# Kernel optimization log

Hardware: AMD Instinct MI355X
Metric: run time of the kernel (lower is better)

## Reference

```python
import jax, jax.numpy as jnp
import numpy as np

B, T, C_IN = 2, 4096, 1024
INTER, OUT = 1024, 1024
ROPE_DIM = 64
GAMMA = 0.99609375  # 1 - 2**-8
GROUPS = 32
EPS = 1e-6


def setup_inputs() -> dict:
    key = jax.random.key(0)
    k = jax.random.split(key, 4)
    return {
        "X_Q": jax.random.normal(k[0], (B, T, C_IN), dtype=jnp.float32),
        "W_Q": jax.random.normal(k[1], (C_IN, INTER), dtype=jnp.float32) / C_IN,
        "W_K": jax.random.normal(k[2], (C_IN, INTER), dtype=jnp.float32) / C_IN,
        "W_V": jax.random.normal(k[3], (C_IN, OUT), dtype=jnp.float32) / C_IN,
        "gn_weight": jnp.ones((OUT,), dtype=jnp.float32),
        "gn_bias": jnp.zeros((OUT,), dtype=jnp.float32),
    }


def _rope(x):
    # lucidrains RotaryEmbedding: rotate first ROPE_DIM features, pairwise-adjacent
    t = x.shape[-2]
    inv_freq = 1.0 / (10000.0 ** (jnp.arange(0, ROPE_DIM, 2, dtype=jnp.float32) / ROPE_DIM))
    freqs = jnp.arange(t, dtype=jnp.float32)[:, None] * inv_freq[None, :]  # [T, ROPE_DIM/2]
    freqs = jnp.repeat(freqs, 2, axis=-1)                                   # [T, ROPE_DIM]
    cos, sin = jnp.cos(freqs), jnp.sin(freqs)
    xr, xp = x[..., :ROPE_DIM], x[..., ROPE_DIM:]
    x1, x2 = xr[..., 0::2], xr[..., 1::2]
    rot = jnp.stack([-x2, x1], axis=-1).reshape(xr.shape)  # rotate_half (adjacent pairs)
    return jnp.concatenate([xr * cos + rot * sin, xp], axis=-1)


def _group_norm(x, w, b):
    # torch GroupNorm applied on x.reshape(-1, C)
    sh = x.shape
    c = sh[-1]
    xr = x.reshape(-1, GROUPS, c // GROUPS)
    mu = xr.mean(-1, keepdims=True)
    var = xr.var(-1, keepdims=True)
    xn = ((xr - mu) * jax.lax.rsqrt(var + EPS)).reshape(-1, c)
    return (xn * w + b).reshape(sh)


def reference(X_Q, W_Q, W_K, W_V, gn_weight, gn_bias):
    Q = jax.nn.silu(_rope(X_Q @ W_Q))  # [B,T,INTER]
    K = jax.nn.silu(_rope(X_Q @ W_K))
    V = jax.nn.silu(X_Q @ W_V)         # [B,T,OUT]
    A = jnp.einsum('btd,bsd->bts', Q, K)  # [B,T,T]
    # decay mask: original multiplies by _get_D(gamma,T).T -> gamma^(m-n) for m>=n
    n = jnp.arange(T)[:, None]
    m = jnp.arange(T)[None, :]
    upper = m >= n
    Dt = jnp.where(upper, GAMMA ** jnp.where(upper, m - n, 0).astype(jnp.float32), 0.0)
    A = A * Dt
    out = jnp.einsum('bts,bsd->btd', A, V)  # [B,T,OUT]
    # dropout p=0 (eval) -> identity
    return _group_norm(out, gn_weight, gn_bias)
```

## Files before the change

### kernel.cpp

```cpp
#include <hip/hip_runtime.h>


typedef __attribute__((ext_vector_type(8))) short bf16x8;
typedef __attribute__((ext_vector_type(4))) short bf16x4;
typedef __attribute__((ext_vector_type(4))) float f32x4;

#define MFMA16(a, b, c) __builtin_amdgcn_mfma_f32_16x16x32_bf16(a, b, c, 0, 0, 0)

static __device__ __forceinline__ short f2bf(float f) {
  unsigned u = __builtin_bit_cast(unsigned, f);
  u = (u + 0x7fffu + ((u >> 16) & 1u)) >> 16;
  return (short)u;
}

static __device__ __forceinline__ void gl_lds16(const void* g, void* l) {
  __builtin_amdgcn_global_load_lds(
      (const __attribute__((address_space(1))) void*)g,
      (__attribute__((address_space(3))) void*)l, 16, 0, 0);
}

static __device__ __forceinline__ int swzc(int col, int row) {
  return (((col >> 3) ^ (row & 7)) << 3) | (col & 7);
}

#define T_LEN 4096
#define CIN 1024

#define LOG2G (-0.0056465633f)
#define L2IF (0.41524101f)

__global__ __launch_bounds__(256)
void convert_x(const float* __restrict__ X, short* __restrict__ Xb) {
  const int gid = blockIdx.x * 256 + threadIdx.x;
  const int row = gid >> 7;
  const int c = gid & 127;
  const float* s = &X[(size_t)gid * 8];
  float4 f0 = *(const float4*)s;
  float4 f1 = *(const float4*)(s + 4);
  bf16x8 v = {f2bf(f0.x), f2bf(f0.y), f2bf(f0.z), f2bf(f0.w),
              f2bf(f1.x), f2bf(f1.y), f2bf(f1.z), f2bf(f1.w)};
  const int pc = (c & 0x78) | ((c ^ row) & 7);
  *(bf16x8*)&Xb[(size_t)row * 1024 + pc * 8] = v;
}

__global__ __launch_bounds__(256)
void transpose_w(const float* __restrict__ Wq, const float* __restrict__ Wk,
                 const float* __restrict__ Wv, short* __restrict__ WT) {
  const int k0 = blockIdx.x * 64, n0 = blockIdx.y * 64, mat = blockIdx.z;
  const float* __restrict__ W = (mat == 0) ? Wq : (mat == 1) ? Wk : Wv;
  __shared__ short tile[64][72];
  const int tid = threadIdx.x;
  const int r = tid >> 4, c = tid & 15;
#pragma unroll
  for (int i = 0; i < 4; ++i) {
    int row = r + 16 * i;
    float4 f = *(const float4*)&W[(size_t)(k0 + row) * CIN + n0 + c * 4];
    tile[c * 4 + 0][row] = f2bf(f.x);
    tile[c * 4 + 1][row] = f2bf(f.y);
    tile[c * 4 + 2][row] = f2bf(f.z);
    tile[c * 4 + 3][row] = f2bf(f.w);
  }
  __syncthreads();
  const int n = tid >> 2, seg = tid & 3;
  bf16x8 lo = *(const bf16x8*)&tile[n][seg * 16];
  bf16x8 hi = *(const bf16x8*)&tile[n][seg * 16 + 8];
  const int R = mat * 1024 + n0 + n;
  const int a0 = (k0 >> 3) + seg * 2;
  short* base = &WT[(size_t)R * CIN];
  *(bf16x8*)&base[(a0 ^ (n & 7)) * 8] = lo;
  *(bf16x8*)&base[((a0 + 1) ^ (n & 7)) * 8] = hi;
}

#define GEMM_DECLS()                                   \
  const int tid = threadIdx.x;                         \
  const int lane = tid & 63, wave = tid >> 6;          \
  const int wm = wave >> 1, wn = wave & 1;             \
  const int l15 = lane & 15, quad = lane >> 4;         \
  const int srow = tid >> 3;                           \
  const int scol = (tid & 7) * 8;                      \
  const int asw = (l15 & 7);

#define ACC_INIT4(acc)                                 \
  _Pragma("unroll") for (int i = 0; i < 4; ++i)        \
  _Pragma("unroll") for (int j = 0; j < 4; ++j) {      \
    f32x4 z = {0.f, 0.f, 0.f, 0.f};                    \
    acc[i][j] = z;                                     \
  }

#define STAGE_TILE(dst, src, ld, r0, k0, nrows)        \
  _Pragma("unroll") for (int i = 0; i < (nrows) / 32; ++i) \
    gl_lds16(&src[(size_t)((r0) + i * 32 + srow) * (ld) + (k0) + scol], \
             &dst[i * 32 + srow][scol]);

#define FRAG_MFMA44(As, Bs, acc)                                            \
  {                                                                         \
    bf16x8 af[4][2], bfr[4][2];                                             \
    _Pragma("unroll") for (int im = 0; im < 4; ++im)                        \
    _Pragma("unroll") for (int ks = 0; ks < 2; ++ks)                        \
      af[im][ks] = *(const bf16x8*)&As[wm * 64 + im * 16 + l15]             \
                       [((ks * 4 + quad) ^ asw) * 8];                       \
    _Pragma("unroll") for (int in = 0; in < 4; ++in)                        \
    _Pragma("unroll") for (int ks = 0; ks < 2; ++ks)                        \
      bfr[in][ks] = *(const bf16x8*)&Bs[wn * 64 + in * 16 + l15]            \
                        [((ks * 4 + quad) ^ asw) * 8];                      \
    _Pragma("unroll") for (int ks = 0; ks < 2; ++ks)                        \
    _Pragma("unroll") for (int im = 0; im < 4; ++im)                        \
    _Pragma("unroll") for (int in = 0; in < 4; ++in)                        \
      acc[im][in] = MFMA16(af[im][ks], bfr[in][ks], acc[im][in]);           \
  }

__global__ __launch_bounds__(256, 2)
void qkv_gemm(const short* __restrict__ Xb, const short* __restrict__ WT,
              short* __restrict__ Qb, short* __restrict__ Kb,
              short* __restrict__ Vt) {
  __shared__ __align__(16) short As[128][64];
  __shared__ __align__(16) short Bs[128][64];
  GEMM_DECLS();
  const int m0 = blockIdx.x * 128;
  const int c0 = blockIdx.y * 128;

  f32x4 acc[4][4];
  ACC_INIT4(acc);

  for (int k0 = 0; k0 < CIN; k0 += 64) {
    __syncthreads();
    STAGE_TILE(As, Xb, CIN, m0, k0, 128);
    STAGE_TILE(Bs, WT, CIN, c0, k0, 128);
    __syncthreads();
    FRAG_MFMA44(As, Bs, acc);
  }

  const int mat = (c0 >> 10);
#pragma unroll
  for (int im = 0; im < 4; ++im) {
#pragma unroll
    for (int in = 0; in < 4; ++in) {
      const int c = c0 + wn * 64 + in * 16 + l15;
      const int colm = c & 1023;
      const bool rope = (mat < 2) && (colm < 64);
      const float invf = exp2f(-L2IF * (float)(colm >> 1));
      const int mbase = m0 + wm * 64 + im * 16 + quad * 4;
      short vv[4];
#pragma unroll
      for (int r = 0; r < 4; ++r) {
        float v = acc[im][in][r];
        int m = mbase + r;
        int t = m & (T_LEN - 1);
        float partner = __shfl_xor(v, 1, 64);
        if (rope) {
          float ang = (float)t * invf;
          float s_, c_;
          sincosf(ang, &s_, &c_);
          v = (colm & 1) ? (v * c_ + partner * s_) : (v * c_ - partner * s_);
        }
        v = v / (1.f + __expf(-v));
        vv[r] = f2bf(v);
      }
      if (mat == 0) {
#pragma unroll
        for (int r = 0; r < 4; ++r)
          Qb[(size_t)(mbase + r) * 1024 + swzc(colm, mbase + r)] = vv[r];
      } else if (mat == 1) {
#pragma unroll
        for (int r = 0; r < 4; ++r)
          Kb[(size_t)(mbase + r) * 1024 + swzc(colm, mbase + r)] = vv[r];
      } else {
        bf16x4 v4 = {vv[0], vv[1], vv[2], vv[3]};
        *(bf16x4*)&Vt[(size_t)colm * 8192 +
                      (((mbase >> 3) ^ (colm & 7)) << 3) + (mbase & 7)] = v4;
      }
    }
  }
}

__global__ __launch_bounds__(256, 2)
void score_kernel(const short* __restrict__ Qb, const short* __restrict__ Kb,
                  short* __restrict__ Ab) {
  int idx = blockIdx.x;
  int ti = 0;
  while (idx >= 32 - ti) { idx -= 32 - ti; ++ti; }
  const int si = ti + idx;
  const int b = blockIdx.y;
  const int s0 = si * 128, t0 = ti * 128;

  __shared__ __align__(16) short Qs[128][64];
  __shared__ __align__(16) short Ks[128][64];
  GEMM_DECLS();

  f32x4 acc[4][4];
  ACC_INIT4(acc);

  for (int k0 = 0; k0 < 1024; k0 += 64) {
    __syncthreads();
    STAGE_TILE(Qs, Qb, 1024, b * T_LEN + t0, k0, 128);
    STAGE_TILE(Ks, Kb, 1024, b * T_LEN + s0, k0, 128);
    __syncthreads();
    FRAG_MFMA44(Qs, Ks, acc);
  }

#pragma unroll
  for (int im = 0; im < 4; ++im) {
#pragma unroll
    for (int in = 0; in < 4; ++in) {
      int s = s0 + wn * 64 + in * 16 + l15;
#pragma unroll
      for (int r = 0; r < 4; ++r) {
        int t = t0 + wm * 64 + im * 16 + quad * 4 + r;
        int d = s - t;
        float v = acc[im][in][r];
        v = (d < 0) ? 0.f : v * exp2f((float)d * LOG2G);
        Ab[((size_t)(b * T_LEN + t)) * T_LEN + swzc(s, t)] = f2bf(v);
      }
    }
  }
}

__global__ __launch_bounds__(256, 2)
void av_kernel(const short* __restrict__ Ab, const short* __restrict__ Vt,
               float* __restrict__ Out) {
  const int p = blockIdx.x, b = blockIdx.y, di = blockIdx.z;
  const int n0 = di * 128;

  __shared__ __align__(16) short As2[64][64];
  __shared__ __align__(16) short Vs[128][64];
  GEMM_DECLS();

#pragma unroll 1
  for (int half = 0; half < 2; ++half) {
    const int ti2 = half ? (63 - p) : p;
    const int t0 = ti2 * 64;

    f32x4 acc[2][4];
#pragma unroll
    for (int i = 0; i < 2; ++i)
#pragma unroll
      for (int j = 0; j < 4; ++j) {
        f32x4 z = {0.f, 0.f, 0.f, 0.f};
        acc[i][j] = z;
      }

    for (int s = t0; s < T_LEN; s += 64) {
      __syncthreads();
      STAGE_TILE(As2, Ab, T_LEN, b * T_LEN + t0, s, 64);
      STAGE_TILE(Vs, Vt, 8192, n0, b * T_LEN + s, 128);
      __syncthreads();
      bf16x8 af[2][2], bfr[4][2];
#pragma unroll
      for (int im = 0; im < 2; ++im)
#pragma unroll
        for (int ks = 0; ks < 2; ++ks)
          af[im][ks] = *(const bf16x8*)&As2[wm * 32 + im * 16 + l15]
                           [((ks * 4 + quad) ^ asw) * 8];
#pragma unroll
      for (int in = 0; in < 4; ++in)
#pragma unroll
        for (int ks = 0; ks < 2; ++ks)
          bfr[in][ks] = *(const bf16x8*)&Vs[wn * 64 + in * 16 + l15]
                            [((ks * 4 + quad) ^ asw) * 8];
#pragma unroll
      for (int ks = 0; ks < 2; ++ks)
#pragma unroll
        for (int im = 0; im < 2; ++im)
#pragma unroll
          for (int in = 0; in < 4; ++in)
            acc[im][in] = MFMA16(af[im][ks], bfr[in][ks], acc[im][in]);
    }

#pragma unroll
    for (int im = 0; im < 2; ++im) {
#pragma unroll
      for (int in = 0; in < 4; ++in) {
        int n = n0 + wn * 64 + in * 16 + l15;
#pragma unroll
        for (int r = 0; r < 4; ++r) {
          int t = t0 + wm * 32 + im * 16 + quad * 4 + r;
          Out[((size_t)(b * T_LEN + t)) * 1024 + n] = acc[im][in][r];
        }
      }
    }
  }
}

__global__ __launch_bounds__(256)
void gn_kernel(float* __restrict__ Out, const float* __restrict__ gw,
               const float* __restrict__ gb) {
  const int row = blockIdx.x;
  const int tid = threadIdx.x;
  const int ch0 = tid * 4;
  float4 v = *(const float4*)&Out[(size_t)row * 1024 + ch0];
  float s = v.x + v.y + v.z + v.w;
  float q = v.x * v.x + v.y * v.y + v.z * v.z + v.w * v.w;
  s += __shfl_xor(s, 1, 64);
  q += __shfl_xor(q, 1, 64);
  s += __shfl_xor(s, 2, 64);
  q += __shfl_xor(q, 2, 64);
  s += __shfl_xor(s, 4, 64);
  q += __shfl_xor(q, 4, 64);
  float mean = s * (1.f / 32.f);
  float var = q * (1.f / 32.f) - mean * mean;
  float rstd = rsqrtf(var + 1e-6f);
  float4 o;
  o.x = (v.x - mean) * rstd * gw[ch0 + 0] + gb[ch0 + 0];
  o.y = (v.y - mean) * rstd * gw[ch0 + 1] + gb[ch0 + 1];
  o.z = (v.z - mean) * rstd * gw[ch0 + 2] + gb[ch0 + 2];
  o.w = (v.w - mean) * rstd * gw[ch0 + 3] + gb[ch0 + 3];
  *(float4*)&Out[(size_t)row * 1024 + ch0] = o;
}

extern "C" void kernel_launch(void* const* d_in, const int* in_sizes, int n_in,
                              void* d_out, int out_size, void* d_ws,
                              size_t ws_size, hipStream_t stream) {
  const float* X = (const float*)d_in[0];
  const float* Wq = (const float*)d_in[1];
  const float* Wk = (const float*)d_in[2];
  const float* Wv = (const float*)d_in[3];
  const float* gw = (const float*)d_in[4];
  const float* gb = (const float*)d_in[5];
  float* Out = (float*)d_out;

  short* Qb = (short*)d_ws;
  short* Kb = Qb + (size_t)8192 * 1024;
  short* Vt = Kb + (size_t)8192 * 1024;
  short* Ab = Vt + (size_t)8192 * 1024;
  short* Xb = Ab;
  short* WT = Xb + (size_t)8192 * 1024;

  convert_x<<<4096, 256, 0, stream>>>(X, Xb);
  transpose_w<<<dim3(16, 16, 3), 256, 0, stream>>>(Wq, Wk, Wv, WT);
  qkv_gemm<<<dim3(64, 24), 256, 0, stream>>>(Xb, WT, Qb, Kb, Vt);
  score_kernel<<<dim3(528, 2), 256, 0, stream>>>(Qb, Kb, Ab);
  av_kernel<<<dim3(32, 2, 8), 256, 0, stream>>>(Ab, Vt, Out);
  gn_kernel<<<8192, 256, 0, stream>>>(Out, gw, gb);
}
```

Baseline: 318.5 us.

## Fuse GroupNorm into AV epilogue, merge prep kernels, use fast rope/silu math

Computes GroupNorm statistics inside the AV kernel epilogue with wave shuffles across the 32-channel group and writes normalized output directly. This removes the separate gn_kernel and its extra read and write of the 32 MB output. It also merges the X conversion and weight transpose into a single launch. In the QKV epilogue it uses the fast __sinf/__cosf and rcp intrinsics, with a block-uniform branch for the rope columns. These intrinsics slightly reduce accuracy for large rope angles.

```diff
diff --git a/kernel.cpp b/kernel.cpp
--- a/kernel.cpp
+++ b/kernel.cpp
@@ -13,6 +13,10 @@
   return (short)u;
 }
 
+static __device__ __forceinline__ float fast_silu(float v) {
+  return v * __builtin_amdgcn_rcpf(1.f + __expf(-v));
+}
+
 static __device__ __forceinline__ void gl_lds16(const void* g, void* l) {
   __builtin_amdgcn_global_load_lds(
       (const __attribute__((address_space(1))) void*)g,
@@ -30,26 +34,28 @@
 #define L2IF (0.41524101f)
 
 __global__ __launch_bounds__(256)
-void convert_x(const float* __restrict__ X, short* __restrict__ Xb) {
-  const int gid = blockIdx.x * 256 + threadIdx.x;
-  const int row = gid >> 7;
-  const int c = gid & 127;
-  const float* s = &X[(size_t)gid * 8];
-  float4 f0 = *(const float4*)s;
-  float4 f1 = *(const float4*)(s + 4);
-  bf16x8 v = {f2bf(f0.x), f2bf(f0.y), f2bf(f0.z), f2bf(f0.w),
-              f2bf(f1.x), f2bf(f1.y), f2bf(f1.z), f2bf(f1.w)};
-  const int pc = (c & 0x78) | ((c ^ row) & 7);
-  *(bf16x8*)&Xb[(size_t)row * 1024 + pc * 8] = v;
-}
-
-__global__ __launch_bounds__(256)
-void transpose_w(const float* __restrict__ Wq, const float* __restrict__ Wk,
+void prep_kernel(const float* __restrict__ X, short* __restrict__ Xb,
+                 const float* __restrict__ Wq, const float* __restrict__ Wk,
                  const float* __restrict__ Wv, short* __restrict__ WT) {
-  const int k0 = blockIdx.x * 64, n0 = blockIdx.y * 64, mat = blockIdx.z;
+  __shared__ short tile[64][72];
+  const int bx = blockIdx.x;
+  const int tid = threadIdx.x;
+  if (bx < 4096) {
+    const int gid = bx * 256 + tid;
+    const int row = gid >> 7;
+    const int c = gid & 127;
+    const float* s = &X[(size_t)gid * 8];
+    float4 f0 = *(const float4*)s;
+    float4 f1 = *(const float4*)(s + 4);
+    bf16x8 v = {f2bf(f0.x), f2bf(f0.y), f2bf(f0.z), f2bf(f0.w),
+                f2bf(f1.x), f2bf(f1.y), f2bf(f1.z), f2bf(f1.w)};
+    const int pc = (c & 0x78) | ((c ^ row) & 7);
+    *(bf16x8*)&Xb[(size_t)row * 1024 + pc * 8] = v;
+    return;
+  }
+  const int bx2 = bx - 4096;
+  const int k0 = (bx2 & 15) * 64, n0 = ((bx2 >> 4) & 15) * 64, mat = bx2 >> 8;
   const float* __restrict__ W = (mat == 0) ? Wq : (mat == 1) ? Wk : Wv;
-  __shared__ short tile[64][72];
-  const int tid = threadIdx.x;
   const int r = tid >> 4, c = tid & 15;
 #pragma unroll
   for (int i = 0; i < 4; ++i) {
@@ -131,30 +137,30 @@
   }
 
   const int mat = (c0 >> 10);
+  const bool ropeBlk = (mat < 2) && ((c0 & 1023) == 0);
 #pragma unroll
   for (int im = 0; im < 4; ++im) {
 #pragma unroll
     for (int in = 0; in < 4; ++in) {
       const int c = c0 + wn * 64 + in * 16 + l15;
       const int colm = c & 1023;
-      const bool rope = (mat < 2) && (colm < 64);
-      const float invf = exp2f(-L2IF * (float)(colm >> 1));
       const int mbase = m0 + wm * 64 + im * 16 + quad * 4;
       short vv[4];
-#pragma unroll
-      for (int r = 0; r < 4; ++r) {
-        float v = acc[im][in][r];
-        int m = mbase + r;
-        int t = m & (T_LEN - 1);
-        float partner = __shfl_xor(v, 1, 64);
-        if (rope) {
+      if (ropeBlk && colm < 64) {
+        const float invf = exp2f(-L2IF * (float)(colm >> 1));
+#pragma unroll
+        for (int r = 0; r < 4; ++r) {
+          float v = acc[im][in][r];
+          int t = (mbase + r) & (T_LEN - 1);
+          float partner = __shfl_xor(v, 1, 64);
           float ang = (float)t * invf;
-          float s_, c_;
-          sincosf(ang, &s_, &c_);
+          float s_ = __sinf(ang), c_ = __cosf(ang);
           v = (colm & 1) ? (v * c_ + partner * s_) : (v * c_ - partner * s_);
+          vv[r] = f2bf(fast_silu(v));
         }
-        v = v / (1.f + __expf(-v));
-        vv[r] = f2bf(v);
+      } else {
+#pragma unroll
+        for (int r = 0; r < 4; ++r) vv[r] = f2bf(fast_silu(acc[im][in][r]));
       }
       if (mat == 0) {
 #pragma unroll
@@ -217,6 +223,7 @@
 
 __global__ __launch_bounds__(256, 2)
 void av_kernel(const short* __restrict__ Ab, const short* __restrict__ Vt,
+               const float* __restrict__ gw, const float* __restrict__ gb,
                float* __restrict__ Out) {
   const int p = blockIdx.x, b = blockIdx.y, di = blockIdx.z;
   const int n0 = di * 128;
@@ -224,6 +231,14 @@
   __shared__ __align__(16) short As2[64][64];
   __shared__ __align__(16) short Vs[128][64];
   GEMM_DECLS();
+
+  float w4[4], b4[4];
+#pragma unroll
+  for (int in = 0; in < 4; ++in) {
+    int n = n0 + wn * 64 + in * 16 + l15;
+    w4[in] = gw[n];
+    b4[in] = gb[n];
+  }
 
 #pragma unroll 1
   for (int half = 0; half < 2; ++half) {
@@ -269,42 +284,32 @@
 #pragma unroll
     for (int im = 0; im < 2; ++im) {
 #pragma unroll
-      for (int in = 0; in < 4; ++in) {
-        int n = n0 + wn * 64 + in * 16 + l15;
-#pragma unroll
-        for (int r = 0; r < 4; ++r) {
-          int t = t0 + wm * 32 + im * 16 + quad * 4 + r;
-          Out[((size_t)(b * T_LEN + t)) * 1024 + n] = acc[im][in][r];
+      for (int r = 0; r < 4; ++r) {
+        int t = t0 + wm * 32 + im * 16 + quad * 4 + r;
+        float* orow = &Out[((size_t)(b * T_LEN + t)) * 1024];
+#pragma unroll
+        for (int g = 0; g < 2; ++g) {
+          float a0 = acc[im][g * 2][r], a1 = acc[im][g * 2 + 1][r];
+          float s = a0 + a1;
+          float q = a0 * a0 + a1 * a1;
+          s += __shfl_xor(s, 1, 64);
+          q += __shfl_xor(q, 1, 64);
+          s += __shfl_xor(s, 2, 64);
+          q += __shfl_xor(q, 2, 64);
+          s += __shfl_xor(s, 4, 64);
+          q += __shfl_xor(q, 4, 64);
+          s += __shfl_xor(s, 8, 64);
+          q += __shfl_xor(q, 8, 64);
+          float mean = s * (1.f / 32.f);
+          float var = q * (1.f / 32.f) - mean * mean;
+          float rstd = rsqrtf(var + 1e-6f);
+          int n = n0 + wn * 64 + g * 32 + l15;
+          orow[n] = (a0 - mean) * rstd * w4[g * 2] + b4[g * 2];
+          orow[n + 16] = (a1 - mean) * rstd * w4[g * 2 + 1] + b4[g * 2 + 1];
         }
       }
     }
   }
-}
-
-__global__ __launch_bounds__(256)
-void gn_kernel(float* __restrict__ Out, const float* __restrict__ gw,
-               const float* __restrict__ gb) {
-  const int row = blockIdx.x;
-  const int tid = threadIdx.x;
-  const int ch0 = tid * 4;
-  float4 v = *(const float4*)&Out[(size_t)row * 1024 + ch0];
-  float s = v.x + v.y + v.z + v.w;
-  float q = v.x * v.x + v.y * v.y + v.z * v.z + v.w * v.w;
-  s += __shfl_xor(s, 1, 64);
-  q += __shfl_xor(q, 1, 64);
-  s += __shfl_xor(s, 2, 64);
-  q += __shfl_xor(q, 2, 64);
-  s += __shfl_xor(s, 4, 64);
-  q += __shfl_xor(q, 4, 64);
-  float mean = s * (1.f / 32.f);
-  float var = q * (1.f / 32.f) - mean * mean;
-  float rstd = rsqrtf(var + 1e-6f);
-  float4 o;
-  o.x = (v.x - mean) * rstd * gw[ch0 + 0] + gb[ch0 + 0];
-  o.y = (v.y - mean) * rstd * gw[ch0 + 1] + gb[ch0 + 1];
-  o.z = (v.z - mean) * rstd * gw[ch0 + 2] + gb[ch0 + 2];
-  o.w = (v.w - mean) * rstd * gw[ch0 + 3] + gb[ch0 + 3];
-  *(float4*)&Out[(size_t)row * 1024 + ch0] = o;
 }
 
 extern "C" void kernel_launch(void* const* d_in, const int* in_sizes, int n_in,
@@ -325,10 +330,8 @@
   short* Xb = Ab;
   short* WT = Xb + (size_t)8192 * 1024;
 
-  convert_x<<<4096, 256, 0, stream>>>(X, Xb);
-  transpose_w<<<dim3(16, 16, 3), 256, 0, stream>>>(Wq, Wk, Wv, WT);
+  prep_kernel<<<4864, 256, 0, stream>>>(X, Xb, Wq, Wk, Wv, WT);
   qkv_gemm<<<dim3(64, 24), 256, 0, stream>>>(Xb, WT, Qb, Kb, Vt);
   score_kernel<<<dim3(528, 2), 256, 0, stream>>>(Qb, Kb, Ab);
-  av_kernel<<<dim3(32, 2, 8), 256, 0, stream>>>(Ab, Vt, Out);
-  gn_kernel<<<8192, 256, 0, stream>>>(Out, gw, gb);
-}
+  av_kernel<<<dim3(32, 2, 8), 256, 0, stream>>>(Ab, Vt, gw, gb, Out);
+}
```

After: 290.2 us. 1.1x faster.
